# Kernel optimization log

Measured on AMD Instinct MI355X. Metric: run time of the kernel, lower is better.

Reference implementation:

```python
import jax, jax.numpy as jnp
import numpy as np
import math

DIM = 1024
HEAD = 16


def setup_inputs() -> dict:
    key = jax.random.key(0)
    k1, k2, k3, k4, k5 = jax.random.split(key, 5)
    scale = 1.0 / math.sqrt(DIM)
    return {
        "x": jax.random.normal(k1, (2, 2048, DIM), dtype=jnp.float32),
        "W_kqv": jax.random.uniform(k2, (3 * DIM, DIM), minval=-scale, maxval=scale, dtype=jnp.float32),
        "b_kqv": jax.random.uniform(k3, (3 * DIM,), minval=-scale, maxval=scale, dtype=jnp.float32),
        "W_out": jax.random.uniform(k4, (DIM, DIM), minval=-scale, maxval=scale, dtype=jnp.float32),
        "b_out": jax.random.uniform(k5, (DIM,), minval=-scale, maxval=scale, dtype=jnp.float32),
    }


def reference(x, W_kqv, b_kqv, W_out, b_out):
    b, s, h = x.shape
    head = HEAD
    d = h // head
    # fused QKV projection (torch Linear: x @ W.T + b)
    kqv = jnp.einsum("bsh,oh->bso", x, W_kqv) + b_kqv  # [b, s, 3h]
    q, k, v = jnp.split(kqv, 3, axis=-1)
    # [b, s, h] -> [b, head, s, d]
    q = q.reshape(b, s, head, d).transpose(0, 2, 1, 3)
    k = k.reshape(b, s, head, d).transpose(0, 2, 1, 3)
    v = v.reshape(b, s, head, d).transpose(0, 2, 1, 3)
    scores = jnp.einsum("bnqd,bnkd->bnqk", q, k) / jnp.sqrt(jnp.float32(d))
    attn = jax.nn.softmax(scores, axis=-1)
    ctx = jnp.einsum("bnqk,bnkd->bnqd", attn, v)  # [b, head, s, d]
    ctx = ctx.transpose(0, 2, 1, 3).reshape(b, s, h)
    return jnp.einsum("bsh,oh->bso", ctx, W_out) + b_out
```

## Files before the change

### kernel.cpp

```cpp
#include <hip/hip_runtime.h>
#include <hip/hip_bf16.h>

#define DIM   1024
#define NHEAD 16
#define HD    64
#define SEQ   2048
#define BATCH 2
#define QKV3  3072

using short8 = __attribute__((ext_vector_type(8))) short;
using f32x4  = __attribute__((ext_vector_type(4))) float;

__device__ inline short f2bf(float f) {
    union { float f; unsigned u; } x; x.f = f;
    const unsigned r = (x.u + 0x7FFFu + ((x.u >> 16) & 1u)) >> 16;
    return (short)r;
}
__device__ inline unsigned pkbf(float a, float b) {
    union { __hip_bfloat162 h; unsigned u; } cv;
    cv.h = __float22bfloat162_rn(make_float2(a, b));
    return cv.u;
}

__device__ __forceinline__ void g2l16(const void* gptr, void* ldsbase) {
    __builtin_amdgcn_global_load_lds(
        (const __attribute__((address_space(1))) unsigned int*)(unsigned long long)gptr,
        (__attribute__((address_space(3))) unsigned int*)(unsigned int)(unsigned long long)ldsbase,
        16, 0, 0);
}

__global__ __launch_bounds__(256)
void conv_bf16(const float* __restrict__ x, const float* __restrict__ wk,
               const float* __restrict__ wo,
               unsigned short* __restrict__ xb, unsigned short* __restrict__ wkb,
               unsigned short* __restrict__ wob)
{
    const int bid = blockIdx.x;
    const float* src; unsigned short* dst; size_t base;
    if (bid < 1024)      { src = x;  dst = xb;  base = (size_t)bid * 4096; }
    else if (bid < 1792) { src = wk; dst = wkb; base = (size_t)(bid - 1024) * 4096; }
    else                 { src = wo; dst = wob; base = (size_t)(bid - 1792) * 4096; }
    const size_t off = base + threadIdx.x * 16;
    const float4 f0 = *(const float4*)(src + off + 0);
    const float4 f1 = *(const float4*)(src + off + 4);
    const float4 f2 = *(const float4*)(src + off + 8);
    const float4 f3 = *(const float4*)(src + off + 12);
    uint4 o0, o1;
    o0.x = pkbf(f0.x, f0.y); o0.y = pkbf(f0.z, f0.w);
    o0.z = pkbf(f1.x, f1.y); o0.w = pkbf(f1.z, f1.w);
    o1.x = pkbf(f2.x, f2.y); o1.y = pkbf(f2.z, f2.w);
    o1.z = pkbf(f3.x, f3.y); o1.w = pkbf(f3.z, f3.w);
    *(uint4*)(dst + off + 0) = o0;
    *(uint4*)(dst + off + 8) = o1;
}

__global__ __launch_bounds__(256)
void gemm_qkv(const unsigned short* __restrict__ A, const unsigned short* __restrict__ B,
              const float* __restrict__ bias,
              unsigned short* __restrict__ qbf, unsigned short* __restrict__ kbf,
              unsigned short* __restrict__ vtbf)
{
    constexpr int BK = 32;
    const int K = DIM;
    __shared__ short As[128 * BK];
    __shared__ short Bs[128 * BK];

    const int tid  = threadIdx.x;
    const int lane = tid & 63;
    const int wave = tid >> 6;
    const int quad = lane >> 4;
    const int ln   = lane & 15;
    const int wm   = (wave & 1) * 64;
    const int wn   = (wave >> 1) * 64;

    const int bid = blockIdx.x;
    const int xcd = bid & 7;
    const int t   = bid >> 3;
    const int m0  = (xcd * 4 + (t & 3)) * 128;
    const int n0  = (t >> 2) * 128;

    int srow[2], sg[2];
#pragma unroll
    for (int i = 0; i < 2; ++i) {
        const int c  = wave * 128 + i * 64 + lane;
        srow[i] = c >> 2;
        sg[i]   = (c & 3) ^ ((srow[i] >> 1) & 3);
    }

    f32x4 acc[4][4];
#pragma unroll
    for (int i = 0; i < 4; ++i)
#pragma unroll
        for (int j = 0; j < 4; ++j) acc[i][j] = (f32x4){0.f, 0.f, 0.f, 0.f};

    for (int k0 = 0; k0 < K; k0 += BK) {
        __syncthreads();
#pragma unroll
        for (int i = 0; i < 2; ++i) {
            const int cb = wave * 128 + i * 64;
            g2l16(A + (size_t)(m0 + srow[i]) * K + k0 + sg[i] * 8, &As[cb * 8]);
            g2l16(B + (size_t)(n0 + srow[i]) * K + k0 + sg[i] * 8, &Bs[cb * 8]);
        }
        __syncthreads();

        short8 a[4], b[4];
#pragma unroll
        for (int i = 0; i < 4; ++i) {
            const int row = wm + i * 16 + ln;
            const int ch  = quad ^ ((row >> 1) & 3);
            a[i] = *(const short8*)&As[row * BK + ch * 8];
        }
#pragma unroll
        for (int j = 0; j < 4; ++j) {
            const int row = wn + j * 16 + ln;
            const int ch  = quad ^ ((row >> 1) & 3);
            b[j] = *(const short8*)&Bs[row * BK + ch * 8];
        }
#pragma unroll
        for (int i = 0; i < 4; ++i)
#pragma unroll
            for (int j = 0; j < 4; ++j)
                acc[i][j] = __builtin_amdgcn_mfma_f32_16x16x32_bf16(
                    a[i], b[j], acc[i][j], 0, 0, 0);
    }

#pragma unroll
    for (int j = 0; j < 4; ++j) {
        const int col = n0 + wn + j * 16 + ln;
        const int sel = col >> 10;
        const int c   = col & 1023;
        const int hh  = c >> 6;
        const int dd  = c & 63;
        const float bv = bias[col];
        if (sel < 2) {
            unsigned short* dst = (sel == 0) ? qbf : kbf;
            const float qs = (sel == 0) ? 0.18033688f : 1.0f;
#pragma unroll
            for (int i = 0; i < 4; ++i)
#pragma unroll
                for (int r2 = 0; r2 < 4; ++r2) {
                    const int row = m0 + wm + i * 16 + quad * 4 + r2;
                    const int bb = row >> 11, ss = row & 2047;
                    dst[((size_t)(bb * NHEAD + hh) * SEQ + ss) * HD + dd] =
                        (unsigned short)f2bf((acc[i][j][r2] + bv) * qs);
                }
        } else {
            const int row0 = m0 + wm + quad * 4;
            const int bb = row0 >> 11;
            const size_t vbase = ((size_t)(bb * NHEAD + hh) * HD + dd) * SEQ;
#pragma unroll
            for (int i = 0; i < 4; ++i) {
                const int ss0 = (row0 & 2047) + i * 16;
                uint2 pk;
                pk.x = pkbf(acc[i][j][0] + bv, acc[i][j][1] + bv);
                pk.y = pkbf(acc[i][j][2] + bv, acc[i][j][3] + bv);
                *(uint2*)&vtbf[vbase + ss0] = pk;
            }
        }
    }
}

__global__ __launch_bounds__(256)
void attn_flash_mfma(const unsigned short* __restrict__ qbf,
                     const unsigned short* __restrict__ kbf,
                     const unsigned short* __restrict__ vtbf,
                     unsigned short* __restrict__ ctxbf)
{
    constexpr int LDP = 72;
    __shared__ short Ks[2][64 * 64];
    __shared__ short Vt[2][64 * 64];
    __shared__ short Ps[128 * LDP];

    const int tid  = threadIdx.x;
    const int lane = tid & 63;
    const int wave = tid >> 6;
    const int quad = lane >> 4;
    const int ln   = lane & 15;

    const int bid = blockIdx.x;
    const int bh  = bid & 31;
    const int qt  = bid >> 5;
    const int q0  = qt * 128;
    const int b   = bh >> 4;
    const int h   = bh & 15;

    const size_t sbase = (size_t)bh * SEQ * HD;
    const size_t vbase = (size_t)bh * HD * SEQ;

    int srw[2], scg[2];
#pragma unroll
    for (int it = 0; it < 2; ++it) {
        const int ch = tid + it * 256;
        srw[it] = ch >> 3;
        scg[it] = (ch & 7) ^ (srw[it] & 7);
    }

#pragma unroll
    for (int it = 0; it < 4; ++it) {
        const int ch = tid + it * 256;
        const int r  = ch >> 3;
        const int cc = ch & 7;
        *(short8*)&Ps[r * LDP + cc * 8] =
            *(const short8*)&qbf[sbase + (size_t)(q0 + r) * HD + cc * 8];
    }
#pragma unroll
    for (int it = 0; it < 2; ++it) {
        const int cb = tid + it * 256;
        g2l16(kbf + sbase + (size_t)srw[it] * HD + scg[it] * 8, &Ks[0][cb * 8]);
        g2l16(vtbf + vbase + (size_t)srw[it] * SEQ + scg[it] * 8, &Vt[0][cb * 8]);
    }
    __syncthreads();

    short8 qf[2][2];
#pragma unroll
    for (int sm = 0; sm < 2; ++sm)
#pragma unroll
        for (int kc = 0; kc < 2; ++kc)
            qf[sm][kc] = *(const short8*)&Ps[(wave * 32 + sm * 16 + ln) * LDP + kc * 32 + quad * 8];

    f32x4 O[2][4];
#pragma unroll
    for (int sm = 0; sm < 2; ++sm)
#pragma unroll
        for (int dj = 0; dj < 4; ++dj) O[sm][dj] = (f32x4){0.f, 0.f, 0.f, 0.f};
    f32x4 lacc[2];
    lacc[0] = (f32x4){0.f, 0.f, 0.f, 0.f};
    lacc[1] = (f32x4){0.f, 0.f, 0.f, 0.f};

    short8 vone;
#pragma unroll
    for (int t = 0; t < 8; ++t) vone[t] = (short)0x3F80;

    for (int kt = 0; kt < SEQ / 64; ++kt) {
        const int p = kt & 1;
        if (kt + 1 < SEQ / 64) {
            const int k0n = (kt + 1) * 64;
#pragma unroll
            for (int it = 0; it < 2; ++it) {
                const int cb = tid + it * 256;
                g2l16(kbf + sbase + (size_t)(k0n + srw[it]) * HD + scg[it] * 8,
                      &Ks[1 - p][cb * 8]);
                g2l16(vtbf + vbase + (size_t)srw[it] * SEQ + k0n + scg[it] * 8,
                      &Vt[1 - p][cb * 8]);
            }
        }

        f32x4 st[2][4];
#pragma unroll
        for (int j = 0; j < 4; ++j) {
            const int row = j * 16 + ln;
            const int c0 = quad ^ (row & 7);
            const int c1 = (4 + quad) ^ (row & 7);
            const short8 kf0 = *(const short8*)&Ks[p][row * 64 + c0 * 8];
            const short8 kf1 = *(const short8*)&Ks[p][row * 64 + c1 * 8];
#pragma unroll
            for (int sm = 0; sm < 2; ++sm) {
                f32x4 tt = __builtin_amdgcn_mfma_f32_16x16x32_bf16(
                    kf0, qf[sm][0], (f32x4){0.f, 0.f, 0.f, 0.f}, 0, 0, 0);
                st[sm][j] = __builtin_amdgcn_mfma_f32_16x16x32_bf16(
                    kf1, qf[sm][1], tt, 0, 0, 0);
            }
        }

#pragma unroll
        for (int sm = 0; sm < 2; ++sm)
#pragma unroll
            for (int j = 0; j < 4; ++j) {
                const float p0 = __builtin_amdgcn_exp2f(st[sm][j][0]);
                const float p1 = __builtin_amdgcn_exp2f(st[sm][j][1]);
                const float p2 = __builtin_amdgcn_exp2f(st[sm][j][2]);
                const float p3 = __builtin_amdgcn_exp2f(st[sm][j][3]);
                uint2 pk;
                pk.x = pkbf(p0, p1);
                pk.y = pkbf(p2, p3);
                *(uint2*)&Ps[(wave * 32 + sm * 16 + ln) * LDP + j * 16 + quad * 4] = pk;
            }

#pragma unroll
        for (int kc = 0; kc < 2; ++kc) {
            const short8 pf0 = *(const short8*)&Ps[(wave * 32 + ln) * LDP + kc * 32 + quad * 8];
            const short8 pf1 = *(const short8*)&Ps[(wave * 32 + 16 + ln) * LDP + kc * 32 + quad * 8];
            lacc[0] = __builtin_amdgcn_mfma_f32_16x16x32_bf16(pf0, vone, lacc[0], 0, 0, 0);
            lacc[1] = __builtin_amdgcn_mfma_f32_16x16x32_bf16(pf1, vone, lacc[1], 0, 0, 0);
#pragma unroll
            for (int dj = 0; dj < 4; ++dj) {
                const int row = dj * 16 + ln;
                const int cg  = (kc * 4 + quad) ^ (row & 7);
                const short8 vf = *(const short8*)&Vt[p][row * 64 + cg * 8];
                O[0][dj] = __builtin_amdgcn_mfma_f32_16x16x32_bf16(pf0, vf, O[0][dj], 0, 0, 0);
                O[1][dj] = __builtin_amdgcn_mfma_f32_16x16x32_bf16(pf1, vf, O[1][dj], 0, 0, 0);
            }
        }
        __syncthreads();
    }

#pragma unroll
    for (int sm = 0; sm < 2; ++sm)
#pragma unroll
        for (int r2 = 0; r2 < 4; ++r2) {
            const float inv = 1.0f / lacc[sm][r2];
            const int row = b * SEQ + q0 + wave * 32 + sm * 16 + quad * 4 + r2;
#pragma unroll
            for (int dj = 0; dj < 4; ++dj)
                ctxbf[(size_t)row * DIM + h * HD + dj * 16 + ln] =
                    (unsigned short)f2bf(O[sm][dj][r2] * inv);
        }
}

__global__ __launch_bounds__(256)
void gemm_out(const unsigned short* __restrict__ A, const unsigned short* __restrict__ B,
              const float* __restrict__ bias, float* __restrict__ C)
{
    constexpr int BK = 32;
    const int K = DIM, N = DIM;
    __shared__ short As[128 * BK];
    __shared__ short Bs[64 * BK];

    const int tid  = threadIdx.x;
    const int lane = tid & 63;
    const int wave = tid >> 6;
    const int quad = lane >> 4;
    const int ln   = lane & 15;
    const int wm   = (wave & 1) * 64;
    const int wn   = (wave >> 1) * 32;

    const int bid = blockIdx.x;
    const int xcd = bid & 7;
    const int t   = bid >> 3;
    const int m0  = (xcd * 4 + (t & 3)) * 128;
    const int n0  = (t >> 2) * 64;

    int srow[2], sg[2];
#pragma unroll
    for (int i = 0; i < 2; ++i) {
        const int c  = wave * 128 + i * 64 + lane;
        srow[i] = c >> 2;
        sg[i]   = (c & 3) ^ ((srow[i] >> 1) & 3);
    }
    const int cB  = wave * 64 + lane;
    const int brow = cB >> 2;
    const int bg   = (cB & 3) ^ ((brow >> 1) & 3);

    f32x4 acc[4][2];
#pragma unroll
    for (int i = 0; i < 4; ++i)
#pragma unroll
        for (int j = 0; j < 2; ++j) acc[i][j] = (f32x4){0.f, 0.f, 0.f, 0.f};

    for (int k0 = 0; k0 < K; k0 += BK) {
        __syncthreads();
#pragma unroll
        for (int i = 0; i < 2; ++i)
            g2l16(A + (size_t)(m0 + srow[i]) * K + k0 + sg[i] * 8,
                  &As[(wave * 128 + i * 64) * 8]);
        g2l16(B + (size_t)(n0 + brow) * K + k0 + bg * 8, &Bs[(wave * 64) * 8]);
        __syncthreads();

        short8 a[4], b[2];
#pragma unroll
        for (int i = 0; i < 4; ++i) {
            const int row = wm + i * 16 + ln;
            const int ch  = quad ^ ((row >> 1) & 3);
            a[i] = *(const short8*)&As[row * BK + ch * 8];
        }
#pragma unroll
        for (int j = 0; j < 2; ++j) {
            const int row = wn + j * 16 + ln;
            const int ch  = quad ^ ((row >> 1) & 3);
            b[j] = *(const short8*)&Bs[row * BK + ch * 8];
        }
#pragma unroll
        for (int i = 0; i < 4; ++i)
#pragma unroll
            for (int j = 0; j < 2; ++j)
                acc[i][j] = __builtin_amdgcn_mfma_f32_16x16x32_bf16(
                    a[i], b[j], acc[i][j], 0, 0, 0);
    }

#pragma unroll
    for (int j = 0; j < 2; ++j) {
        const int col = n0 + wn + j * 16 + ln;
        const float bv = bias[col];
#pragma unroll
        for (int i = 0; i < 4; ++i)
#pragma unroll
            for (int r2 = 0; r2 < 4; ++r2) {
                const int row = m0 + wm + i * 16 + quad * 4 + r2;
                C[(size_t)row * N + col] = acc[i][j][r2] + bv;
            }
    }
}

extern "C" void kernel_launch(void* const* d_in, const int* in_sizes, int n_in,
                              void* d_out, int out_size, void* d_ws, size_t ws_size,
                              hipStream_t stream)
{
    const float* x     = (const float*)d_in[0];
    const float* W_kqv = (const float*)d_in[1];
    const float* b_kqv = (const float*)d_in[2];
    const float* W_out = (const float*)d_in[3];
    const float* b_out = (const float*)d_in[4];
    float* out = (float*)d_out;

    char* w = (char*)d_ws;
    unsigned short* qbf   = (unsigned short*)w;  w += (size_t)BATCH * NHEAD * SEQ * HD * 2;
    unsigned short* kbf   = (unsigned short*)w;  w += (size_t)BATCH * NHEAD * SEQ * HD * 2;
    unsigned short* vtbf  = (unsigned short*)w;  w += (size_t)BATCH * NHEAD * HD * SEQ * 2;
    unsigned short* ctxbf = (unsigned short*)w;  w += (size_t)BATCH * SEQ * DIM * 2;
    unsigned short* xb    = (unsigned short*)w;  w += (size_t)BATCH * SEQ * DIM * 2;
    unsigned short* wkb   = (unsigned short*)w;  w += (size_t)QKV3 * DIM * 2;
    unsigned short* wob   = (unsigned short*)w;

    dim3 blk(256);

    conv_bf16<<<dim3(2048), blk, 0, stream>>>(x, W_kqv, W_out, xb, wkb, wob);

    gemm_qkv<<<dim3(768), blk, 0, stream>>>(xb, wkb, b_kqv, qbf, kbf, vtbf);

    attn_flash_mfma<<<dim3(512), blk, 0, stream>>>(qbf, kbf, vtbf, ctxbf);

    gemm_out<<<dim3(512), blk, 0, stream>>>(ctxbf, wob, b_out, out);
}
```

Measured before the change: 205.3 us.

## Double-buffer LDS tiles in QKV and output projection GEMMs

After: 191.1 us. 1.07x faster.

```diff
diff --git a/kernel.cpp b/kernel.cpp
--- a/kernel.cpp
+++ b/kernel.cpp
@@ -60,10 +60,10 @@
               unsigned short* __restrict__ qbf, unsigned short* __restrict__ kbf,
               unsigned short* __restrict__ vtbf)
 {
-    constexpr int BK = 32;
+    constexpr int BK = 32, NIT = DIM / BK;
     const int K = DIM;
-    __shared__ short As[128 * BK];
-    __shared__ short Bs[128 * BK];
+    __shared__ short As[2][128 * BK];
+    __shared__ short Bs[2][128 * BK];
 
     const int tid  = threadIdx.x;
     const int lane = tid & 63;
@@ -93,28 +93,38 @@
 #pragma unroll
         for (int j = 0; j < 4; ++j) acc[i][j] = (f32x4){0.f, 0.f, 0.f, 0.f};
 
-    for (int k0 = 0; k0 < K; k0 += BK) {
-        __syncthreads();
-#pragma unroll
-        for (int i = 0; i < 2; ++i) {
-            const int cb = wave * 128 + i * 64;
-            g2l16(A + (size_t)(m0 + srow[i]) * K + k0 + sg[i] * 8, &As[cb * 8]);
-            g2l16(B + (size_t)(n0 + srow[i]) * K + k0 + sg[i] * 8, &Bs[cb * 8]);
-        }
-        __syncthreads();
+#pragma unroll
+    for (int i = 0; i < 2; ++i) {
+        const int cb = wave * 128 + i * 64;
+        g2l16(A + (size_t)(m0 + srow[i]) * K + sg[i] * 8, &As[0][cb * 8]);
+        g2l16(B + (size_t)(n0 + srow[i]) * K + sg[i] * 8, &Bs[0][cb * 8]);
+    }
+    __syncthreads();
+
+    for (int kt = 0; kt < NIT; ++kt) {
+        const int p = kt & 1;
+        if (kt + 1 < NIT) {
+            const int kn = (kt + 1) * BK;
+#pragma unroll
+            for (int i = 0; i < 2; ++i) {
+                const int cb = wave * 128 + i * 64;
+                g2l16(A + (size_t)(m0 + srow[i]) * K + kn + sg[i] * 8, &As[1 - p][cb * 8]);
+                g2l16(B + (size_t)(n0 + srow[i]) * K + kn + sg[i] * 8, &Bs[1 - p][cb * 8]);
+            }
+        }
 
         short8 a[4], b[4];
 #pragma unroll
         for (int i = 0; i < 4; ++i) {
             const int row = wm + i * 16 + ln;
             const int ch  = quad ^ ((row >> 1) & 3);
-            a[i] = *(const short8*)&As[row * BK + ch * 8];
+            a[i] = *(const short8*)&As[p][row * BK + ch * 8];
         }
 #pragma unroll
         for (int j = 0; j < 4; ++j) {
             const int row = wn + j * 16 + ln;
             const int ch  = quad ^ ((row >> 1) & 3);
-            b[j] = *(const short8*)&Bs[row * BK + ch * 8];
+            b[j] = *(const short8*)&Bs[p][row * BK + ch * 8];
         }
 #pragma unroll
         for (int i = 0; i < 4; ++i)
@@ -122,6 +132,7 @@
             for (int j = 0; j < 4; ++j)
                 acc[i][j] = __builtin_amdgcn_mfma_f32_16x16x32_bf16(
                     a[i], b[j], acc[i][j], 0, 0, 0);
+        __syncthreads();
     }
 
 #pragma unroll
@@ -311,10 +322,10 @@
 void gemm_out(const unsigned short* __restrict__ A, const unsigned short* __restrict__ B,
               const float* __restrict__ bias, float* __restrict__ C)
 {
-    constexpr int BK = 32;
+    constexpr int BK = 32, NIT = DIM / BK;
     const int K = DIM, N = DIM;
-    __shared__ short As[128 * BK];
-    __shared__ short Bs[64 * BK];
+    __shared__ short As[2][128 * BK];
+    __shared__ short Bs[2][64 * BK];
 
     const int tid  = threadIdx.x;
     const int lane = tid & 63;
@@ -347,27 +358,36 @@
 #pragma unroll
         for (int j = 0; j < 2; ++j) acc[i][j] = (f32x4){0.f, 0.f, 0.f, 0.f};
 
-    for (int k0 = 0; k0 < K; k0 += BK) {
-        __syncthreads();
-#pragma unroll
-        for (int i = 0; i < 2; ++i)
-            g2l16(A + (size_t)(m0 + srow[i]) * K + k0 + sg[i] * 8,
-                  &As[(wave * 128 + i * 64) * 8]);
-        g2l16(B + (size_t)(n0 + brow) * K + k0 + bg * 8, &Bs[(wave * 64) * 8]);
-        __syncthreads();
+#pragma unroll
+    for (int i = 0; i < 2; ++i)
+        g2l16(A + (size_t)(m0 + srow[i]) * K + sg[i] * 8,
+              &As[0][(wave * 128 + i * 64) * 8]);
+    g2l16(B + (size_t)(n0 + brow) * K + bg * 8, &Bs[0][(wave * 64) * 8]);
+    __syncthreads();
+
+    for (int kt = 0; kt < NIT; ++kt) {
+        const int p = kt & 1;
+        if (kt + 1 < NIT) {
+            const int kn = (kt + 1) * BK;
+#pragma unroll
+            for (int i = 0; i < 2; ++i)
+                g2l16(A + (size_t)(m0 + srow[i]) * K + kn + sg[i] * 8,
+                      &As[1 - p][(wave * 128 + i * 64) * 8]);
+            g2l16(B + (size_t)(n0 + brow) * K + kn + bg * 8, &Bs[1 - p][(wave * 64) * 8]);
+        }
 
         short8 a[4], b[2];
 #pragma unroll
         for (int i = 0; i < 4; ++i) {
             const int row = wm + i * 16 + ln;
             const int ch  = quad ^ ((row >> 1) & 3);
-            a[i] = *(const short8*)&As[row * BK + ch * 8];
+            a[i] = *(const short8*)&As[p][row * BK + ch * 8];
         }
 #pragma unroll
         for (int j = 0; j < 2; ++j) {
             const int row = wn + j * 16 + ln;
             const int ch  = quad ^ ((row >> 1) & 3);
-            b[j] = *(const short8*)&Bs[row * BK + ch * 8];
+            b[j] = *(const short8*)&Bs[p][row * BK + ch * 8];
         }
 #pragma unroll
         for (int i = 0; i < 4; ++i)
@@ -375,6 +395,7 @@
             for (int j = 0; j < 2; ++j)
                 acc[i][j] = __builtin_amdgcn_mfma_f32_16x16x32_bf16(
                     a[i], b[j], acc[i][j], 0, 0, 0);
+        __syncthreads();
     }
 
 #pragma unroll
```
